# Kernel tuning notes

Measured on AMD Instinct MI355X. Metric: run time of the kernel, lower is better.

Reference implementation:

```python
import jax, jax.numpy as jnp
import numpy as np

D_MODEL = 1024
D_INNER = 4096   # expand=4
D_STATE = 16
D_CONV = 4
DT_RANK = 64     # ceil(d_model/16)
BATCH = 2
SEQLEN = 2048


def setup_inputs() -> dict:
    key = jax.random.key(0)
    ks = jax.random.split(key, 9)
    s = 0.02
    x = jax.random.normal(ks[0], (BATCH, SEQLEN, D_MODEL), jnp.float32)
    in_proj_w = jax.random.normal(ks[1], (D_MODEL, 2 * D_INNER), jnp.float32) * s
    conv_w = jax.random.normal(ks[2], (D_INNER, D_CONV), jnp.float32) * 0.3
    conv_b = jax.random.normal(ks[3], (D_INNER,), jnp.float32) * 0.02
    x_proj_w = jax.random.normal(ks[4], (D_INNER, DT_RANK + 2 * D_STATE), jnp.float32) * s
    dt_proj_w = jax.random.normal(ks[5], (DT_RANK, D_INNER), jnp.float32) * (DT_RANK ** -0.5)
    dt_proj_b = jax.random.normal(ks[6], (D_INNER,), jnp.float32) * 0.1 - 4.0  # small softplus(dt)
    # A = repeat(arange(1, d_state+1)) as in mamba-ssm; A_log = log(A)
    A_log = jnp.log(jnp.broadcast_to(jnp.arange(1, D_STATE + 1, dtype=jnp.float32), (D_INNER, D_STATE)))
    D = jnp.ones((D_INNER,), jnp.float32)
    out_proj_w = jax.random.normal(ks[7], (D_INNER, D_MODEL), jnp.float32) * s
    return {"x": x, "in_proj_w": in_proj_w, "conv_w": conv_w, "conv_b": conv_b,
            "x_proj_w": x_proj_w, "dt_proj_w": dt_proj_w, "dt_proj_b": dt_proj_b,
            "A_log": A_log, "D": D, "out_proj_w": out_proj_w}


def reference(x, in_proj_w, conv_w, conv_b, x_proj_w, dt_proj_w, dt_proj_b, A_log, D, out_proj_w):
    Bsz, L, _ = x.shape
    # input projection -> (x branch, gate z), each [B, L, d_inner]
    xz = x @ in_proj_w
    xc, z = jnp.split(xz, 2, axis=-1)
    # causal depthwise conv1d, kernel D_CONV, left-padded
    xp = jnp.pad(xc, ((0, 0), (D_CONV - 1, 0), (0, 0)))
    xconv = conv_b + sum(xp[:, k:k + L, :] * conv_w[:, k] for k in range(D_CONV))
    xs = jax.nn.silu(xconv)  # [B, L, d_inner]
    # input-dependent SSM params
    proj = xs @ x_proj_w  # [B, L, dt_rank + 2*d_state]
    dt_lo, Bt, Ct = jnp.split(proj, [DT_RANK, DT_RANK + D_STATE], axis=-1)
    dt = jax.nn.softplus(dt_lo @ dt_proj_w + dt_proj_b)  # [B, L, d_inner]
    A = -jnp.exp(A_log)  # [d_inner, d_state]

    def step(h, inp):
        dt_t, B_t, C_t, u_t = inp  # [B,dI], [B,dS], [B,dS], [B,dI]
        dA = jnp.exp(dt_t[..., None] * A)                       # [B, dI, dS]
        h = h * dA + (dt_t * u_t)[..., None] * B_t[:, None, :]  # [B, dI, dS]
        y = jnp.einsum('bdn,bn->bd', h, C_t)                    # [B, dI]
        return h, y

    h0 = jnp.zeros((Bsz, D_INNER, D_STATE), x.dtype)
    inps = (dt.transpose(1, 0, 2), Bt.transpose(1, 0, 2),
            Ct.transpose(1, 0, 2), xs.transpose(1, 0, 2))
    _, ys = jax.lax.scan(step, h0, inps)  # ys: [L, B, d_inner]
    y = ys.transpose(1, 0, 2) + xs * D
    y = y * jax.nn.silu(z)
    return y @ out_proj_w
```

## Files before the change

kernel.cpp:

```cpp
#include <hip/hip_runtime.h>
#include <hip/hip_bf16.h>

#define D_MODEL 1024
#define D_INNER 4096
#define D_STATE 16
#define D_CONV 4
#define DT_RANK 64
#define BATCH 2
#define SEQLEN 2048
#define MROWS (BATCH * SEQLEN)
#define NPROJ (DT_RANK + 2 * D_STATE)
#define PST 128
#define NC 32
#define TC (SEQLEN / NC)
#define KSPLIT 8
#define KSP6 4

typedef unsigned short u16;
typedef unsigned int u32;
typedef __attribute__((ext_vector_type(8))) short short8;
typedef __attribute__((ext_vector_type(4))) float floatx4;

#define LOG2E 1.44269504089f

__device__ __forceinline__ float bf2f(u16 u) {
    union { u32 i; float f; } v; v.i = ((u32)u) << 16; return v.f;
}
__device__ __forceinline__ u16 f2bf(float f) {
    union { float f; u32 i; } v; v.f = f;
    u32 x = v.i;
    u32 r = x + 0x7fffu + ((x >> 16) & 1u);
    return (u16)(r >> 16);
}
__device__ __forceinline__ float softplus_fast(float x) {
    float l = __logf(1.f + __expf(-fabsf(x)));
    return x > 0.f ? x + l : l;
}
__device__ __forceinline__ float sigmoid_fast(float x) {
    return __builtin_amdgcn_rcpf(1.f + __expf(-x));
}
__device__ __forceinline__ float exp2_hw(float x) {
    float r;
    asm("v_exp_f32 %0, %1" : "=v"(r) : "v"(x));
    return r;
}
__device__ __forceinline__ void pow_tree16(float r, float* pw) {
    pw[0] = r;
    pw[1] = r * r;
    pw[2] = pw[1] * r;
    pw[3] = pw[1] * pw[1];
    pw[4] = pw[3] * r;
    pw[5] = pw[3] * pw[1];
    pw[6] = pw[3] * pw[2];
    pw[7] = pw[3] * pw[3];
#pragma unroll
    for (int k = 0; k < 8; k++) pw[8 + k] = pw[7] * pw[k];
}
__device__ __forceinline__ void async_cp16(const u16* g, u16* l) {
    __builtin_amdgcn_global_load_lds((const __attribute__((address_space(1))) void*)g,
                                     (__attribute__((address_space(3))) void*)l, 16, 0, 0);
}

__global__ __launch_bounds__(256) void detect_dtype(const u16* __restrict__ x, int* __restrict__ flag,
                                                    int* __restrict__ sflag) {
    __shared__ int cnt;
    if (threadIdx.x == 0) { cnt = 0; *sflag = 0; }
    __syncthreads();
    int local = 0;
    for (int k = 0; k < 16; k++) {
        int e = threadIdx.x * 8192 + k * 512;
        u16 v = x[2 * e];
        int ex = (v >> 7) & 0xFF;
        if (ex >= 0x68 && ex <= 0x8F) local++;
    }
    atomicAdd(&cnt, local);
    __syncthreads();
    if (threadIdx.x == 0) *flag = (cnt >= 2458) ? 1 : 0;
}

__global__ __launch_bounds__(256) void ingest16(const void* __restrict__ src, u16* __restrict__ dst,
                                                int n, const int* __restrict__ flag) {
    int i = blockIdx.x * 256 + threadIdx.x;
    if (i >= n) return;
    if (*flag) dst[i] = ((const u16*)src)[i];
    else       dst[i] = f2bf(((const float*)src)[i]);
}

__global__ __launch_bounds__(256) void prep_small(const void* __restrict__ cw, const void* __restrict__ cb,
                                                  const void* __restrict__ dtb, const void* __restrict__ Dv,
                                                  const void* __restrict__ Alog,
                                                  u16* __restrict__ cw16, u16* __restrict__ cb16,
                                                  u16* __restrict__ dtb16, u16* __restrict__ D16,
                                                  float* __restrict__ A, const int* __restrict__ flag,
                                                  int* __restrict__ sflag) {
    int i = blockIdx.x * 256 + threadIdx.x;
    int isb = *flag;
    if (i < D_INNER * D_CONV)
        cw16[i] = isb ? ((const u16*)cw)[i] : f2bf(((const float*)cw)[i]);
    if (i < D_INNER) {
        cb16[i]  = isb ? ((const u16*)cb)[i]  : f2bf(((const float*)cb)[i]);
        dtb16[i] = isb ? ((const u16*)dtb)[i] : f2bf(((const float*)dtb)[i]);
        D16[i]   = isb ? ((const u16*)Dv)[i]  : f2bf(((const float*)Dv)[i]);
    }
    if (i < D_INNER * D_STATE) {
        float v = isb ? bf2f(((const u16*)Alog)[i]) : ((const float*)Alog)[i];
        float a = -expf(v);
        A[i] = a;
        float tgt = (float)((i & 15) + 1);
        if (fabsf(a + tgt) > 4e-6f * tgt) atomicOr(sflag, 1);
    }
}

__global__ __launch_bounds__(256) void transpose_w(const void* __restrict__ W, u16* __restrict__ WT,
                                                   int K, int N, const int* __restrict__ flag) {
    __shared__ float t[32][33];
    int k0 = blockIdx.y * 32, n0 = blockIdx.x * 32;
    int tid = threadIdx.x;
    int r = tid >> 3, c4 = (tid & 7) * 4;
    int isb = *flag;
    size_t base = (size_t)(k0 + r) * N + n0 + c4;
    float4 v;
    if (isb) { ushort4 u4 = *(const ushort4*)((const u16*)W + base);
               v = make_float4(bf2f(u4.x), bf2f(u4.y), bf2f(u4.z), bf2f(u4.w)); }
    else     { v = *(const float4*)((const float*)W + base); }
    t[c4 + 0][r] = v.x; t[c4 + 1][r] = v.y; t[c4 + 2][r] = v.z; t[c4 + 3][r] = v.w;
    __syncthreads();
    u16* o = WT + (size_t)(n0 + r) * K + k0 + c4;
    o[0] = f2bf(t[r][c4 + 0]);
    o[1] = f2bf(t[r][c4 + 1]);
    o[2] = f2bf(t[r][c4 + 2]);
    o[3] = f2bf(t[r][c4 + 3]);
}

template<int KS, int MODE>
__global__ __launch_bounds__(512, 2) void gemm8p(const u16* __restrict__ A, const u16* __restrict__ Bt,
                                                 u16* __restrict__ o0, u16* __restrict__ o1,
                                                 float* __restrict__ Pp) {
    __shared__ __align__(16) u16 lds[65536];
    const int tid = threadIdx.x;
    const int lane = tid & 63;
    const int wave = tid >> 6;
    const int wr = wave >> 2, wc = wave & 3;
    const int quad = lane >> 4, l15 = lane & 15;

    int m0, n0, kbase, kz;
    if (MODE == 0) {
        int wgid = (blockIdx.x & 7) * 64 + (blockIdx.x >> 3);
        m0 = (wgid & 15) * 256;
        n0 = (wgid >> 4) * 256;
        kbase = 0; kz = 0;
    } else {
        m0 = blockIdx.y * 256;
        n0 = blockIdx.x * 256;
        kz = blockIdx.z;
        kbase = kz * 1024;
    }
    const int NT = 1024 / 64;

    const int srow = tid >> 3;
    const int kswz = (((tid & 7) ^ (srow & 7)) << 3);
    const u16* pA = A + (size_t)(m0 + srow) * KS + kbase + kswz;
    const u16* pB = Bt + (size_t)(n0 + srow) * KS + kbase + kswz;

    const int rsw = (l15 & 7) << 3;
    const int ksel0 = (quad * 8) ^ rsw;
    const int ksel1 = (32 + quad * 8) ^ rsw;
    const int aoff = (wr * 64 + l15) * 64;
    const int boff = (wc * 32 + l15) * 64;

    floatx4 acc[8][4];
#pragma unroll
    for (int i = 0; i < 8; i++)
#pragma unroll
        for (int j = 0; j < 4; j++) acc[i][j] = (floatx4)0.f;
    short8 af[4][2];
    short8 bf[2][2][2];

#define STAGE_A(nb, h, kt) do { \
    const u16* g_ = pA + (size_t)(h) * 128 * KS + (kt) * 64; \
    u16* l_ = &lds[((nb) * 2 + (h)) * 8192 + tid * 8]; \
    async_cp16(g_, l_); \
    async_cp16(g_ + (size_t)64 * KS, l_ + 4096); \
} while (0)
#define STAGE_B(nb, h, kt) do { \
    const u16* g_ = pB + (size_t)(h) * 128 * KS + (kt) * 64; \
    u16* l_ = &lds[32768 + ((nb) * 2 + (h)) * 8192 + tid * 8]; \
    async_cp16(g_, l_); \
    async_cp16(g_ + (size_t)64 * KS, l_ + 4096); \
} while (0)
#define LOADA(b, h) do { \
    const u16* p_ = &lds[((b) * 2 + (h)) * 8192 + aoff]; \
    _Pragma("unroll") \
    for (int ii = 0; ii < 4; ii++) { \
        af[ii][0] = *(const short8*)(p_ + ii * 1024 + ksel0); \
        af[ii][1] = *(const short8*)(p_ + ii * 1024 + ksel1); \
    } \
} while (0)
#define LOADB(b, h) do { \
    const u16* p_ = &lds[32768 + ((b) * 2 + (h)) * 8192 + boff]; \
    _Pragma("unroll") \
    for (int jj = 0; jj < 2; jj++) { \
        bf[h][jj][0] = *(const short8*)(p_ + jj * 1024 + ksel0); \
        bf[h][jj][1] = *(const short8*)(p_ + jj * 1024 + ksel1); \
    } \
} while (0)
#define MFMAQ(qa, qb) do { \
    __builtin_amdgcn_s_setprio(1); \
    _Pragma("unroll") \
    for (int ii = 0; ii < 4; ii++) \
    _Pragma("unroll") \
    for (int jj = 0; jj < 2; jj++) { \
        floatx4 c_ = acc[(qa) * 4 + ii][(qb) * 2 + jj]; \
        c_ = __builtin_amdgcn_mfma_f32_16x16x32_bf16(af[ii][0], bf[qb][jj][0], c_, 0, 0, 0); \
        c_ = __builtin_amdgcn_mfma_f32_16x16x32_bf16(af[ii][1], bf[qb][jj][1], c_, 0, 0, 0); \
        acc[(qa) * 4 + ii][(qb) * 2 + jj] = c_; \
    } \
    __builtin_amdgcn_s_setprio(0); \
} while (0)
#define VMW(N) asm volatile("s_waitcnt vmcnt(" #N ")" ::: "memory")
#define BARX() do { __builtin_amdgcn_s_barrier(); asm volatile("" ::: "memory"); } while (0)
#define SANDWICH() do { \
    __builtin_amdgcn_sched_barrier(0); \
    __builtin_amdgcn_s_barrier(); \
    asm volatile("s_waitcnt lgkmcnt(0)" ::: "memory"); \
    __builtin_amdgcn_sched_barrier(0); \
} while (0)

    STAGE_A(0, 0, 0);
    STAGE_B(0, 0, 0);
    STAGE_B(0, 1, 0);
    STAGE_A(0, 1, 0);
    VMW(4); BARX();

    for (int t = 0; t < NT - 1; ++t) {
        const int b = t & 1, nb = b ^ 1;
        LOADA(b, 0);
        LOADB(b, 0);
        STAGE_A(nb, 0, t + 1);
        SANDWICH();
        MFMAQ(0, 0);
        VMW(4); BARX();
        LOADB(b, 1);
        STAGE_B(nb, 0, t + 1);
        SANDWICH();
        MFMAQ(0, 1);
        VMW(4); BARX();
        LOADA(b, 1);
        STAGE_B(nb, 1, t + 1);
        SANDWICH();
        MFMAQ(1, 1);
        STAGE_A(nb, 1, t + 1);
        MFMAQ(1, 0);
        VMW(4); BARX();
    }
    {
        const int b = (NT - 1) & 1;
        LOADA(b, 0);
        LOADB(b, 0);
        SANDWICH();
        MFMAQ(0, 0);
        VMW(2); BARX();
        LOADB(b, 1);
        SANDWICH();
        MFMAQ(0, 1);
        VMW(0); BARX();
        LOADA(b, 1);
        MFMAQ(1, 1);
        MFMAQ(1, 0);
    }

    if constexpr (MODE == 0) {
        (void)kz; (void)Pp;
        u16* d = (n0 < D_INNER) ? o0 : o1;
        const int nb0 = (n0 < D_INNER) ? n0 : n0 - D_INNER;
#pragma unroll
        for (int i = 0; i < 8; i++) {
            const int mrow = m0 + wr * 64 + (i & 3) * 16 + (i >> 2) * 128 + quad * 4;
#pragma unroll
            for (int j = 0; j < 4; j++) {
                const int ncol = nb0 + wc * 32 + (j & 1) * 16 + (j >> 1) * 128 + l15;
#pragma unroll
                for (int r = 0; r < 4; r++)
                    d[(size_t)(mrow + r) * D_INNER + ncol] = f2bf(acc[i][j][r]);
            }
        }
    } else {
        (void)o0; (void)o1;
        float* d = Pp + (size_t)kz * MROWS * D_MODEL;
#pragma unroll
        for (int i = 0; i < 8; i++) {
            const int mrow = m0 + wr * 64 + (i & 3) * 16 + (i >> 2) * 128 + quad * 4;
#pragma unroll
            for (int j = 0; j < 4; j++) {
                const int ncol = n0 + wc * 32 + (j & 1) * 16 + (j >> 1) * 128 + l15;
#pragma unroll
                for (int r = 0; r < 4; r++)
                    d[(size_t)(mrow + r) * D_MODEL + ncol] = acc[i][j][r];
            }
        }
    }
#undef STAGE_A
#undef STAGE_B
#undef LOADA
#undef LOADB
#undef MFMAQ
#undef VMW
#undef BARX
#undef SANDWICH
}

__global__ __launch_bounds__(256) void reduce_out(const float* __restrict__ Pp, void* __restrict__ out,
                                                  const int* __restrict__ flag) {
    int i = blockIdx.x * 256 + threadIdx.x;
    float s = 0.f;
#pragma unroll
    for (int z = 0; z < KSP6; z++) s += Pp[(size_t)z * MROWS * D_MODEL + i];
    if (*flag) ((u16*)out)[i] = f2bf(s);
    else       ((float*)out)[i] = s;
}

__global__ __launch_bounds__(256) void gemm_proj(const u16* __restrict__ A, const u16* __restrict__ Bt,
                                                 float* __restrict__ Pp) {
    const int K = D_INNER;
    __shared__ __align__(16) u16 sA[128 * 32];
    __shared__ __align__(16) u16 sB[128 * 32];
    int tid = threadIdx.x;
    int lane = tid & 63;
    int wave = tid >> 6;
    int wm = (wave >> 1) * 64, wn = (wave & 1) * 64;
    int quad = lane >> 4, l15 = lane & 15;
    int m0 = blockIdx.y * 128;
    int kz = blockIdx.x;
    int kbase = kz * (K / KSPLIT);

    floatx4 acc[4][4];
#pragma unroll
    for (int i = 0; i < 4; i++)
#pragma unroll
        for (int j = 0; j < 4; j++) acc[i][j] = (floatx4)0.f;

    const u16* ga0 = A + (size_t)(m0 + (tid >> 2)) * K + (tid & 3) * 8;
    const u16* ga1 = A + (size_t)(m0 + 64 + (tid >> 2)) * K + (tid & 3) * 8;
    const u16* gb0 = Bt + (size_t)(tid >> 2) * K + (tid & 3) * 8;
    const u16* gb1 = Bt + (size_t)(64 + (tid >> 2)) * K + (tid & 3) * 8;
    u16* la0 = &sA[tid * 8];
    u16* la1 = &sA[(256 + tid) * 8];
    u16* lb0 = &sB[tid * 8];
    u16* lb1 = &sB[(256 + tid) * 8];

    for (int k0 = kbase; k0 < kbase + K / KSPLIT; k0 += 32) {
        async_cp16(ga0 + k0, la0);
        async_cp16(ga1 + k0, la1);
        async_cp16(gb0 + k0, lb0);
        async_cp16(gb1 + k0, lb1);
        __syncthreads();
        short8 af[4], bf[4];
#pragma unroll
        for (int i = 0; i < 4; i++) {
            af[i] = *(const short8*)&sA[(wm + i * 16 + l15) * 32 + quad * 8];
            bf[i] = *(const short8*)&sB[(wn + i * 16 + l15) * 32 + quad * 8];
        }
#pragma unroll
        for (int i = 0; i < 4; i++)
#pragma unroll
            for (int j = 0; j < 4; j++)
                acc[i][j] = __builtin_amdgcn_mfma_f32_16x16x32_bf16(af[i], bf[j], acc[i][j], 0, 0, 0);
        __syncthreads();
    }

    float* d = Pp + (size_t)kz * MROWS * PST;
#pragma unroll
    for (int i = 0; i < 4; i++)
#pragma unroll
        for (int j = 0; j < 4; j++)
#pragma unroll
            for (int r = 0; r < 4; r++) {
                int mm = m0 + wm + i * 16 + quad * 4 + r;
                int nn = wn + j * 16 + l15;
                d[(size_t)mm * PST + nn] = acc[i][j][r];
            }
}

__global__ __launch_bounds__(256) void reduce_proj(const float* __restrict__ Pp, float* __restrict__ proj,
                                                   u16* __restrict__ proj_lo) {
    int i = blockIdx.x * 256 + threadIdx.x;
    float s = 0.f;
#pragma unroll
    for (int z = 0; z < KSPLIT; z++) s += Pp[(size_t)z * MROWS * PST + i];
    proj[i] = s;
    int col = i & (PST - 1);
    if (col < DT_RANK) proj_lo[(size_t)(i >> 7) * DT_RANK + col] = f2bf(s);
}

__global__ __launch_bounds__(256) void gemm_dt(const u16* __restrict__ A, const u16* __restrict__ Bt,
                                               const u16* __restrict__ dtb, u16* __restrict__ dt) {
    const int K = DT_RANK;
    __shared__ __align__(16) u16 smem[64 * 132];
    u16* sA = smem;
    u16* sB = smem + 128 * 32;
    int tid = threadIdx.x;
    int lane = tid & 63;
    int wave = tid >> 6;
    int wm = (wave >> 1) * 64, wn = (wave & 1) * 64;
    int quad = lane >> 4, l15 = lane & 15;
    int m0 = blockIdx.y * 128, n0 = blockIdx.x * 128;

    floatx4 acc[4][4];
#pragma unroll
    for (int i = 0; i < 4; i++)
#pragma unroll
        for (int j = 0; j < 4; j++) acc[i][j] = (floatx4)0.f;

    const u16* ga0 = A + (size_t)(m0 + (tid >> 2)) * K + (tid & 3) * 8;
    const u16* ga1 = A + (size_t)(m0 + 64 + (tid >> 2)) * K + (tid & 3) * 8;
    const u16* gb0 = Bt + (size_t)(n0 + (tid >> 2)) * K + (tid & 3) * 8;
    const u16* gb1 = Bt + (size_t)(n0 + 64 + (tid >> 2)) * K + (tid & 3) * 8;
    u16* la0 = &sA[tid * 8];
    u16* la1 = &sA[(256 + tid) * 8];
    u16* lb0 = &sB[tid * 8];
    u16* lb1 = &sB[(256 + tid) * 8];

    for (int k0 = 0; k0 < K; k0 += 32) {
        async_cp16(ga0 + k0, la0);
        async_cp16(ga1 + k0, la1);
        async_cp16(gb0 + k0, lb0);
        async_cp16(gb1 + k0, lb1);
        __syncthreads();
        short8 af[4], bf[4];
#pragma unroll
        for (int i = 0; i < 4; i++) {
            af[i] = *(const short8*)&sA[(wm + i * 16 + l15) * 32 + quad * 8];
            bf[i] = *(const short8*)&sB[(wn + i * 16 + l15) * 32 + quad * 8];
        }
#pragma unroll
        for (int i = 0; i < 4; i++)
#pragma unroll
            for (int j = 0; j < 4; j++)
                acc[i][j] = __builtin_amdgcn_mfma_f32_16x16x32_bf16(af[i], bf[j], acc[i][j], 0, 0, 0);
        __syncthreads();
    }

#pragma unroll
    for (int h = 0; h < 2; h++) {
        __syncthreads();
        if (wm == h * 64) {
#pragma unroll
            for (int j = 0; j < 4; j++) {
                int col = wn + j * 16 + l15;
                float b = bf2f(dtb[n0 + col]);
#pragma unroll
                for (int i = 0; i < 4; i++)
#pragma unroll
                    for (int r = 0; r < 4; r++) {
                        int row = i * 16 + quad * 4 + r;
                        smem[row * 132 + col] = f2bf(softplus_fast(acc[i][j][r] + b));
                    }
            }
        }
        __syncthreads();
#pragma unroll
        for (int p = 0; p < 4; p++) {
            int row = p * 16 + (tid >> 4);
            int chunk = tid & 15;
            uint4 v = *(const uint4*)&smem[row * 132 + chunk * 8];
            *(uint4*)&dt[(size_t)(m0 + h * 64 + row) * D_INNER + n0 + chunk * 8] = v;
        }
    }
}

__global__ __launch_bounds__(256) void conv_silu(const u16* __restrict__ xc, const u16* __restrict__ cw,
                                                 const u16* __restrict__ cb, u16* __restrict__ xs) {
    int idx = blockIdx.x * 256 + threadIdx.x;
    int d = idx & (D_INNER - 1);
    int t = (idx >> 12) & (SEQLEN - 1);
    int b = idx >> 23;
    float w0 = bf2f(cw[d * 4 + 0]), w1 = bf2f(cw[d * 4 + 1]);
    float w2 = bf2f(cw[d * 4 + 2]), w3 = bf2f(cw[d * 4 + 3]);
    float acc = bf2f(cb[d]);
    size_t base = (size_t)b * SEQLEN * D_INNER + d;
    if (t >= 3) acc += bf2f(xc[base + (size_t)(t - 3) * D_INNER]) * w0;
    if (t >= 2) acc += bf2f(xc[base + (size_t)(t - 2) * D_INNER]) * w1;
    if (t >= 1) acc += bf2f(xc[base + (size_t)(t - 1) * D_INNER]) * w2;
    acc += bf2f(xc[base + (size_t)t * D_INNER]) * w3;
    xs[idx] = f2bf(acc * sigmoid_fast(acc));
}

__global__ __launch_bounds__(256) void scan_phase1(const float* __restrict__ proj, const u16* __restrict__ dt,
                                                   const float* __restrict__ A, const u16* __restrict__ xs,
                                                   float* __restrict__ hloc, float* __restrict__ Ssum,
                                                   const int* __restrict__ sflag) {
    int d = blockIdx.x * 256 + threadIdx.x;
    int c = blockIdx.y, b = blockIdx.z;
    int t0 = c * TC;
    int structured = (*sflag == 0);
    float h[16];
#pragma unroll
    for (int n = 0; n < 16; n++) h[n] = 0.f;
    float S = 0.f;
    size_t base = ((size_t)b * SEQLEN + t0) * D_INNER + d;
    const float* prow = proj + ((size_t)b * SEQLEN + t0) * PST + DT_RANK;
    u16 dcur = dt[base], ucur = xs[base];
    if (structured) {
        for (int t = 0; t < TC; t++) {
            size_t nidx = base + (size_t)((t + 1 < TC) ? t + 1 : t) * D_INNER;
            u16 dnxt = dt[nidx];
            u16 unxt = xs[nidx];
            float4 B0 = *(const float4*)(prow + t * PST + 0);
            float4 B1 = *(const float4*)(prow + t * PST + 4);
            float4 B2 = *(const float4*)(prow + t * PST + 8);
            float4 B3 = *(const float4*)(prow + t * PST + 12);
            float dtv = bf2f(dcur), u = bf2f(ucur);
            S += dtv;
            float du = dtv * u;
            float Bf[16] = {B0.x, B0.y, B0.z, B0.w, B1.x, B1.y, B1.z, B1.w,
                            B2.x, B2.y, B2.z, B2.w, B3.x, B3.y, B3.z, B3.w};
            float pw[16];
            pow_tree16(exp2_hw(-LOG2E * dtv), pw);
#pragma unroll
            for (int n = 0; n < 16; n++)
                h[n] = h[n] * pw[n] + du * Bf[n];
            dcur = dnxt; ucur = unxt;
        }
    } else {
        float Areg[16];
        const float4* Ap = (const float4*)(A + (size_t)d * 16);
#pragma unroll
        for (int n = 0; n < 4; n++) {
            float4 v = Ap[n];
            Areg[n * 4 + 0] = v.x * LOG2E; Areg[n * 4 + 1] = v.y * LOG2E;
            Areg[n * 4 + 2] = v.z * LOG2E; Areg[n * 4 + 3] = v.w * LOG2E;
        }
        for (int t = 0; t < TC; t++) {
            size_t nidx = base + (size_t)((t + 1 < TC) ? t + 1 : t) * D_INNER;
            u16 dnxt = dt[nidx];
            u16 unxt = xs[nidx];
            float4 B0 = *(const float4*)(prow + t * PST + 0);
            float4 B1 = *(const float4*)(prow + t * PST + 4);
            float4 B2 = *(const float4*)(prow + t * PST + 8);
            float4 B3 = *(const float4*)(prow + t * PST + 12);
            float dtv = bf2f(dcur), u = bf2f(ucur);
            S += dtv;
            float du = dtv * u;
            float Bf[16] = {B0.x, B0.y, B0.z, B0.w, B1.x, B1.y, B1.z, B1.w,
                            B2.x, B2.y, B2.z, B2.w, B3.x, B3.y, B3.z, B3.w};
#pragma unroll
            for (int n = 0; n < 16; n++)
                h[n] = h[n] * exp2_hw(dtv * Areg[n]) + du * Bf[n];
            dcur = dnxt; ucur = unxt;
        }
    }
    float* hp = &hloc[(((size_t)b * NC + c) * D_INNER + d) * 16];
#pragma unroll
    for (int n = 0; n < 16; n += 4)
        *(float4*)&hp[n] = make_float4(h[n], h[n + 1], h[n + 2], h[n + 3]);
    Ssum[((size_t)b * NC + c) * D_INNER + d] = S;
}

__global__ __launch_bounds__(256) void scan_phase2(const float* __restrict__ A, const float* __restrict__ Ssum,
                                                   float* __restrict__ hloc) {
    int tid = blockIdx.x * 256 + threadIdx.x;
    int n = tid & 15;
    int d = (tid >> 4) & (D_INNER - 1);
    int b = tid >> 16;
    float An2 = A[d * 16 + n] * LOG2E;
    float h = 0.f;
    for (int c = 0; c < NC; c++) {
        size_t idx = (((size_t)b * NC + c) * D_INNER + d) * 16 + n;
        float hl = hloc[idx];
        float S = Ssum[((size_t)b * NC + c) * D_INNER + d];
        hloc[idx] = h;
        h = hl + h * exp2_hw(An2 * S);
    }
}

__global__ __launch_bounds__(256) void scan_phase3(const float* __restrict__ proj, const u16* __restrict__ dt,
                                                   const float* __restrict__ A, const u16* __restrict__ D16,
                                                   const float* __restrict__ hinit, const u16* __restrict__ z16,
                                                   u16* __restrict__ xs, const int* __restrict__ sflag) {
    int d = blockIdx.x * 256 + threadIdx.x;
    int c = blockIdx.y, b = blockIdx.z;
    int t0 = c * TC;
    int structured = (*sflag == 0);
    float h[16];
    {
        const float* hp = &hinit[(((size_t)b * NC + c) * D_INNER + d) * 16];
#pragma unroll
        for (int n = 0; n < 16; n += 4) {
            float4 v = *(const float4*)&hp[n];
            h[n] = v.x; h[n + 1] = v.y; h[n + 2] = v.z; h[n + 3] = v.w;
        }
    }
    float Dd = bf2f(D16[d]);
    size_t base = ((size_t)b * SEQLEN + t0) * D_INNER + d;
    const float* prow = proj + ((size_t)b * SEQLEN + t0) * PST + DT_RANK;
    u16 dcur = dt[base], ucur = xs[base], zcur = z16[base];
    if (structured) {
        for (int t = 0; t < TC; t++) {
            size_t nidx = base + (size_t)((t + 1 < TC) ? t + 1 : t) * D_INNER;
            u16 dnxt = dt[nidx];
            u16 unxt = xs[nidx];
            u16 znxt = z16[nidx];
            float4 B0 = *(const float4*)(prow + t * PST + 0);
            float4 B1 = *(const float4*)(prow + t * PST + 4);
            float4 B2 = *(const float4*)(prow + t * PST + 8);
            float4 B3 = *(const float4*)(prow + t * PST + 12);
            float4 C0 = *(const float4*)(prow + t * PST + 16);
            float4 C1 = *(const float4*)(prow + t * PST + 20);
            float4 C2 = *(const float4*)(prow + t * PST + 24);
            float4 C3 = *(const float4*)(prow + t * PST + 28);
            float dtv = bf2f(dcur), u = bf2f(ucur), zv = bf2f(zcur);
            float du = dtv * u;
            float Bf[16] = {B0.x, B0.y, B0.z, B0.w, B1.x, B1.y, B1.z, B1.w,
                            B2.x, B2.y, B2.z, B2.w, B3.x, B3.y, B3.z, B3.w};
            float Cf[16] = {C0.x, C0.y, C0.z, C0.w, C1.x, C1.y, C1.z, C1.w,
                            C2.x, C2.y, C2.z, C2.w, C3.x, C3.y, C3.z, C3.w};
            float pw[16];
            pow_tree16(exp2_hw(-LOG2E * dtv), pw);
            float y = 0.f;
#pragma unroll
            for (int n = 0; n < 16; n++) {
                h[n] = h[n] * pw[n] + du * Bf[n];
                y += h[n] * Cf[n];
            }
            float gate = zv * sigmoid_fast(zv);
            xs[base + (size_t)t * D_INNER] = f2bf((y + u * Dd) * gate);
            dcur = dnxt; ucur = unxt; zcur = znxt;
        }
    } else {
        float Areg[16];
        const float4* Ap = (const float4*)(A + (size_t)d * 16);
#pragma unroll
        for (int n = 0; n < 4; n++) {
            float4 v = Ap[n];
            Areg[n * 4 + 0] = v.x * LOG2E; Areg[n * 4 + 1] = v.y * LOG2E;
            Areg[n * 4 + 2] = v.z * LOG2E; Areg[n * 4 + 3] = v.w * LOG2E;
        }
        for (int t = 0; t < TC; t++) {
            size_t nidx = base + (size_t)((t + 1 < TC) ? t + 1 : t) * D_INNER;
            u16 dnxt = dt[nidx];
            u16 unxt = xs[nidx];
            u16 znxt = z16[nidx];
            float4 B0 = *(const float4*)(prow + t * PST + 0);
            float4 B1 = *(const float4*)(prow + t * PST + 4);
            float4 B2 = *(const float4*)(prow + t * PST + 8);
            float4 B3 = *(const float4*)(prow + t * PST + 12);
            float4 C0 = *(const float4*)(prow + t * PST + 16);
            float4 C1 = *(const float4*)(prow + t * PST + 20);
            float4 C2 = *(const float4*)(prow + t * PST + 24);
            float4 C3 = *(const float4*)(prow + t * PST + 28);
            float dtv = bf2f(dcur), u = bf2f(ucur), zv = bf2f(zcur);
            float du = dtv * u;
            float Bf[16] = {B0.x, B0.y, B0.z, B0.w, B1.x, B1.y, B1.z, B1.w,
                            B2.x, B2.y, B2.z, B2.w, B3.x, B3.y, B3.z, B3.w};
            float Cf[16] = {C0.x, C0.y, C0.z, C0.w, C1.x, C1.y, C1.z, C1.w,
                            C2.x, C2.y, C2.z, C2.w, C3.x, C3.y, C3.z, C3.w};
            float y = 0.f;
#pragma unroll
            for (int n = 0; n < 16; n++) {
                h[n] = h[n] * exp2_hw(dtv * Areg[n]) + du * Bf[n];
                y += h[n] * Cf[n];
            }
            float gate = zv * sigmoid_fast(zv);
            xs[base + (size_t)t * D_INNER] = f2bf((y + u * Dd) * gate);
            dcur = dnxt; ucur = unxt; zcur = znxt;
        }
    }
}

extern "C" void kernel_launch(void* const* d_in, const int* in_sizes, int n_in,
                              void* d_out, int out_size, void* d_ws, size_t ws_size,
                              hipStream_t stream) {
    const void* x          = d_in[0];
    const void* in_proj_w  = d_in[1];
    const void* conv_w     = d_in[2];
    const void* conv_b     = d_in[3];
    const void* x_proj_w   = d_in[4];
    const void* dt_proj_w  = d_in[5];
    const void* dt_proj_b  = d_in[6];
    const void* A_log      = d_in[7];
    const void* Dvec       = d_in[8];
    const void* out_proj_w = d_in[9];

    char* w = (char*)d_ws;
    const size_t MB = 1024 * 1024;
    const size_t KB = 1024;
    int*   flag    = (int*)(w + 0);
    int*   sflag   = (int*)(w + 16);
    float* Aws     = (float*)(w + 1 * KB);
    float* proj    = (float*)(w + 1 * MB);
    u16*   cw16    = (u16*)(w + 3 * MB);
    u16*   cb16    = (u16*)(w + 3 * MB + 64 * KB);
    u16*   dtb16   = (u16*)(w + 3 * MB + 128 * KB);
    u16*   D16     = (u16*)(w + 3 * MB + 192 * KB);
    u16*   proj_lo = (u16*)(w + 3 * MB + 512 * KB);
    u16*   dtwT    = (u16*)(w + 4 * MB);
    u16*   buf1    = (u16*)(w + 5 * MB);
    u16*   dt16    = buf1;
    u16*   zbuf    = (u16*)(w + 37 * MB);
    float* Pp6     = (float*)(w + 5 * MB);
    u16*   xs      = (u16*)(w + 69 * MB);
    u16*   x16     = (u16*)(w + 101 * MB);
    u16*   ipwT    = (u16*)(w + 110 * MB);
    float* Pp      = (float*)(w + 101 * MB);
    float* hloc    = (float*)(w + 101 * MB);
    float* Ssum    = (float*)(w + 117 * MB);
    u16*   opwT    = (u16*)(w + 127 * MB);
    u16*   xpwT    = (u16*)(w + 136 * MB);

    detect_dtype<<<dim3(1), dim3(256), 0, stream>>>((const u16*)x, flag, sflag);
    prep_small<<<dim3(256), dim3(256), 0, stream>>>(conv_w, conv_b, dt_proj_b, Dvec, A_log,
                                                    cw16, cb16, dtb16, D16, Aws, flag, sflag);
    ingest16<<<dim3(MROWS * D_MODEL / 256), dim3(256), 0, stream>>>(x, x16, MROWS * D_MODEL, flag);
    transpose_w<<<dim3(2 * D_INNER / 32, D_MODEL / 32), dim3(256), 0, stream>>>(in_proj_w, ipwT, D_MODEL, 2 * D_INNER, flag);
    transpose_w<<<dim3(D_MODEL / 32, D_INNER / 32), dim3(256), 0, stream>>>(out_proj_w, opwT, D_INNER, D_MODEL, flag);
    transpose_w<<<dim3(NPROJ / 32, D_INNER / 32), dim3(256), 0, stream>>>(x_proj_w, xpwT, D_INNER, NPROJ, flag);
    transpose_w<<<dim3(D_INNER / 32, DT_RANK / 32), dim3(256), 0, stream>>>(dt_proj_w, dtwT, DT_RANK, D_INNER, flag);

    gemm8p<1024, 0><<<dim3(512), dim3(512), 0, stream>>>(x16, ipwT, buf1, zbuf, nullptr);
    conv_silu<<<dim3(MROWS * D_INNER / 256), dim3(256), 0, stream>>>(buf1, cw16, cb16, xs);
    gemm_proj<<<dim3(KSPLIT, MROWS / 128), dim3(256), 0, stream>>>(xs, xpwT, Pp);
    reduce_proj<<<dim3(MROWS * PST / 256), dim3(256), 0, stream>>>(Pp, proj, proj_lo);
    gemm_dt<<<dim3(D_INNER / 128, MROWS / 128), dim3(256), 0, stream>>>(proj_lo, dtwT, dtb16, dt16);
    scan_phase1<<<dim3(D_INNER / 256, NC, BATCH), dim3(256), 0, stream>>>(proj, dt16, Aws, xs, hloc, Ssum, sflag);
    scan_phase2<<<dim3(BATCH * D_INNER * D_STATE / 256), dim3(256), 0, stream>>>(Aws, Ssum, hloc);
    scan_phase3<<<dim3(D_INNER / 256, NC, BATCH), dim3(256), 0, stream>>>(proj, dt16, Aws, D16, hloc, zbuf, xs, sflag);
    gemm8p<4096, 1><<<dim3(D_MODEL / 256, MROWS / 256, KSP6), dim3(512), 0, stream>>>(xs, opwT, nullptr, nullptr, Pp6);
    reduce_out<<<dim3(MROWS * D_MODEL / 256), dim3(256), 0, stream>>>(Pp6, d_out, flag);
}
```

Before: 461.1 us.

## Switch GEMM to 32x32x16 MFMA and vectorize conv and reduce kernels

The main GEMM kernel now uses 32x32x16 bf16 MFMA instructions with 16-float accumulators instead of 16x16x32, so each wave needs fewer LDS fragment loads per unit of compute. The LDS fragment addressing and epilogue index mapping are rewritten to match the new instruction layout. Separately, conv_silu now handles 8 channels per thread with 128-bit loads and stores, and reduce_out processes 4 elements per thread with float4 accesses. The new layout carries a risk of indexing errors, and the epilogue stores stay strided per lane.

```diff
diff --git a/kernel.cpp b/kernel.cpp
--- a/kernel.cpp
+++ b/kernel.cpp
@@ -20,6 +20,7 @@
 typedef unsigned int u32;
 typedef __attribute__((ext_vector_type(8))) short short8;
 typedef __attribute__((ext_vector_type(4))) float floatx4;
+typedef __attribute__((ext_vector_type(16))) float floatx16;
 
 #define LOG2E 1.44269504089f
 
@@ -141,7 +142,7 @@
     const int lane = tid & 63;
     const int wave = tid >> 6;
     const int wr = wave >> 2, wc = wave & 3;
-    const int quad = lane >> 4, l15 = lane & 15;
+    const int l31 = lane & 31, lhi = lane >> 5, sw = lane & 7;
 
     int m0, n0, kbase, kz;
     if (MODE == 0) {
@@ -162,19 +163,20 @@
     const u16* pA = A + (size_t)(m0 + srow) * KS + kbase + kswz;
     const u16* pB = Bt + (size_t)(n0 + srow) * KS + kbase + kswz;
 
-    const int rsw = (l15 & 7) << 3;
-    const int ksel0 = (quad * 8) ^ rsw;
-    const int ksel1 = (32 + quad * 8) ^ rsw;
-    const int aoff = (wr * 64 + l15) * 64;
-    const int boff = (wc * 32 + l15) * 64;
-
-    floatx4 acc[8][4];
-#pragma unroll
-    for (int i = 0; i < 8; i++)
-#pragma unroll
-        for (int j = 0; j < 4; j++) acc[i][j] = (floatx4)0.f;
-    short8 af[4][2];
-    short8 bf[2][2][2];
+    const int k0f = (((0 + lhi) ^ sw) << 3);
+    const int k1f = (((2 + lhi) ^ sw) << 3);
+    const int k2f = (((4 + lhi) ^ sw) << 3);
+    const int k3f = (((6 + lhi) ^ sw) << 3);
+    const int aoff = (wr * 64 + l31) * 64;
+    const int boff = (wc * 32 + l31) * 64;
+
+    floatx16 acc[4][2];
+#pragma unroll
+    for (int i = 0; i < 4; i++)
+#pragma unroll
+        for (int j = 0; j < 2; j++) acc[i][j] = (floatx16)0.f;
+    short8 af[2][4];
+    short8 bfr[2][4];
 
 #define STAGE_A(nb, h, kt) do { \
     const u16* g_ = pA + (size_t)(h) * 128 * KS + (kt) * 64; \
@@ -190,30 +192,32 @@
 } while (0)
 #define LOADA(b, h) do { \
     const u16* p_ = &lds[((b) * 2 + (h)) * 8192 + aoff]; \
-    _Pragma("unroll") \
-    for (int ii = 0; ii < 4; ii++) { \
-        af[ii][0] = *(const short8*)(p_ + ii * 1024 + ksel0); \
-        af[ii][1] = *(const short8*)(p_ + ii * 1024 + ksel1); \
-    } \
+    af[0][0] = *(const short8*)(p_ + k0f); \
+    af[0][1] = *(const short8*)(p_ + k1f); \
+    af[0][2] = *(const short8*)(p_ + k2f); \
+    af[0][3] = *(const short8*)(p_ + k3f); \
+    af[1][0] = *(const short8*)(p_ + 2048 + k0f); \
+    af[1][1] = *(const short8*)(p_ + 2048 + k1f); \
+    af[1][2] = *(const short8*)(p_ + 2048 + k2f); \
+    af[1][3] = *(const short8*)(p_ + 2048 + k3f); \
 } while (0)
 #define LOADB(b, h) do { \
     const u16* p_ = &lds[32768 + ((b) * 2 + (h)) * 8192 + boff]; \
-    _Pragma("unroll") \
-    for (int jj = 0; jj < 2; jj++) { \
-        bf[h][jj][0] = *(const short8*)(p_ + jj * 1024 + ksel0); \
-        bf[h][jj][1] = *(const short8*)(p_ + jj * 1024 + ksel1); \
-    } \
+    bfr[h][0] = *(const short8*)(p_ + k0f); \
+    bfr[h][1] = *(const short8*)(p_ + k1f); \
+    bfr[h][2] = *(const short8*)(p_ + k2f); \
+    bfr[h][3] = *(const short8*)(p_ + k3f); \
 } while (0)
 #define MFMAQ(qa, qb) do { \
     __builtin_amdgcn_s_setprio(1); \
     _Pragma("unroll") \
-    for (int ii = 0; ii < 4; ii++) \
-    _Pragma("unroll") \
-    for (int jj = 0; jj < 2; jj++) { \
-        floatx4 c_ = acc[(qa) * 4 + ii][(qb) * 2 + jj]; \
-        c_ = __builtin_amdgcn_mfma_f32_16x16x32_bf16(af[ii][0], bf[qb][jj][0], c_, 0, 0, 0); \
-        c_ = __builtin_amdgcn_mfma_f32_16x16x32_bf16(af[ii][1], bf[qb][jj][1], c_, 0, 0, 0); \
-        acc[(qa) * 4 + ii][(qb) * 2 + jj] = c_; \
+    for (int ii = 0; ii < 2; ii++) { \
+        floatx16 c_ = acc[(qa) * 2 + ii][qb]; \
+        c_ = __builtin_amdgcn_mfma_f32_32x32x16_bf16(af[ii][0], bfr[qb][0], c_, 0, 0, 0); \
+        c_ = __builtin_amdgcn_mfma_f32_32x32x16_bf16(af[ii][1], bfr[qb][1], c_, 0, 0, 0); \
+        c_ = __builtin_amdgcn_mfma_f32_32x32x16_bf16(af[ii][2], bfr[qb][2], c_, 0, 0, 0); \
+        c_ = __builtin_amdgcn_mfma_f32_32x32x16_bf16(af[ii][3], bfr[qb][3], c_, 0, 0, 0); \
+        acc[(qa) * 2 + ii][qb] = c_; \
     } \
     __builtin_amdgcn_s_setprio(0); \
 } while (0)
@@ -274,28 +278,32 @@
         u16* d = (n0 < D_INNER) ? o0 : o1;
         const int nb0 = (n0 < D_INNER) ? n0 : n0 - D_INNER;
 #pragma unroll
-        for (int i = 0; i < 8; i++) {
-            const int mrow = m0 + wr * 64 + (i & 3) * 16 + (i >> 2) * 128 + quad * 4;
-#pragma unroll
-            for (int j = 0; j < 4; j++) {
-                const int ncol = nb0 + wc * 32 + (j & 1) * 16 + (j >> 1) * 128 + l15;
-#pragma unroll
-                for (int r = 0; r < 4; r++)
-                    d[(size_t)(mrow + r) * D_INNER + ncol] = f2bf(acc[i][j][r]);
+        for (int i = 0; i < 4; i++) {
+            const int rbase = m0 + (i >> 1) * 128 + wr * 64 + (i & 1) * 32 + lhi * 4;
+#pragma unroll
+            for (int j = 0; j < 2; j++) {
+                const int ncol = nb0 + j * 128 + wc * 32 + l31;
+#pragma unroll
+                for (int reg = 0; reg < 16; reg++) {
+                    const int row = rbase + (reg & 3) + ((reg >> 2) << 3);
+                    d[(size_t)row * D_INNER + ncol] = f2bf(acc[i][j][reg]);
+                }
             }
         }
     } else {
         (void)o0; (void)o1;
         float* d = Pp + (size_t)kz * MROWS * D_MODEL;
 #pragma unroll
-        for (int i = 0; i < 8; i++) {
-            const int mrow = m0 + wr * 64 + (i & 3) * 16 + (i >> 2) * 128 + quad * 4;
-#pragma unroll
-            for (int j = 0; j < 4; j++) {
-                const int ncol = n0 + wc * 32 + (j & 1) * 16 + (j >> 1) * 128 + l15;
-#pragma unroll
-                for (int r = 0; r < 4; r++)
-                    d[(size_t)(mrow + r) * D_MODEL + ncol] = acc[i][j][r];
+        for (int i = 0; i < 4; i++) {
+            const int rbase = m0 + (i >> 1) * 128 + wr * 64 + (i & 1) * 32 + lhi * 4;
+#pragma unroll
+            for (int j = 0; j < 2; j++) {
+                const int ncol = n0 + j * 128 + wc * 32 + l31;
+#pragma unroll
+                for (int reg = 0; reg < 16; reg++) {
+                    const int row = rbase + (reg & 3) + ((reg >> 2) << 3);
+                    d[(size_t)row * D_MODEL + ncol] = acc[i][j][reg];
+                }
             }
         }
     }
@@ -311,12 +319,19 @@
 
 __global__ __launch_bounds__(256) void reduce_out(const float* __restrict__ Pp, void* __restrict__ out,
                                                   const int* __restrict__ flag) {
-    int i = blockIdx.x * 256 + threadIdx.x;
-    float s = 0.f;
-#pragma unroll
-    for (int z = 0; z < KSP6; z++) s += Pp[(size_t)z * MROWS * D_MODEL + i];
-    if (*flag) ((u16*)out)[i] = f2bf(s);
-    else       ((float*)out)[i] = s;
+    int i = (blockIdx.x * 256 + threadIdx.x) * 4;
+    float4 s = *(const float4*)&Pp[i];
+#pragma unroll
+    for (int z = 1; z < KSP6; z++) {
+        float4 p = *(const float4*)&Pp[(size_t)z * MROWS * D_MODEL + i];
+        s.x += p.x; s.y += p.y; s.z += p.z; s.w += p.w;
+    }
+    if (*flag) {
+        ushort4 o = make_ushort4(f2bf(s.x), f2bf(s.y), f2bf(s.z), f2bf(s.w));
+        *(ushort4*)((u16*)out + i) = o;
+    } else {
+        *(float4*)((float*)out + i) = s;
+    }
 }
 
 __global__ __launch_bounds__(256) void gemm_proj(const u16* __restrict__ A, const u16* __restrict__ Bt,
@@ -471,18 +486,37 @@
 __global__ __launch_bounds__(256) void conv_silu(const u16* __restrict__ xc, const u16* __restrict__ cw,
                                                  const u16* __restrict__ cb, u16* __restrict__ xs) {
     int idx = blockIdx.x * 256 + threadIdx.x;
-    int d = idx & (D_INNER - 1);
-    int t = (idx >> 12) & (SEQLEN - 1);
-    int b = idx >> 23;
-    float w0 = bf2f(cw[d * 4 + 0]), w1 = bf2f(cw[d * 4 + 1]);
-    float w2 = bf2f(cw[d * 4 + 2]), w3 = bf2f(cw[d * 4 + 3]);
-    float acc = bf2f(cb[d]);
-    size_t base = (size_t)b * SEQLEN * D_INNER + d;
-    if (t >= 3) acc += bf2f(xc[base + (size_t)(t - 3) * D_INNER]) * w0;
-    if (t >= 2) acc += bf2f(xc[base + (size_t)(t - 2) * D_INNER]) * w1;
-    if (t >= 1) acc += bf2f(xc[base + (size_t)(t - 1) * D_INNER]) * w2;
-    acc += bf2f(xc[base + (size_t)t * D_INNER]) * w3;
-    xs[idx] = f2bf(acc * sigmoid_fast(acc));
+    int g = idx & (D_INNER / 8 - 1);
+    int bt = idx >> 9;
+    int t = bt & (SEQLEN - 1);
+    int d0 = g * 8;
+    size_t row = (size_t)bt * D_INNER + d0;
+    u16 wv[32];
+    *(uint4*)&wv[0]  = *(const uint4*)&cw[d0 * 4];
+    *(uint4*)&wv[8]  = *(const uint4*)&cw[d0 * 4 + 8];
+    *(uint4*)&wv[16] = *(const uint4*)&cw[d0 * 4 + 16];
+    *(uint4*)&wv[24] = *(const uint4*)&cw[d0 * 4 + 24];
+    u16 cbv[8];
+    *(uint4*)&cbv[0] = *(const uint4*)&cb[d0];
+    u16 x0[8] = {0, 0, 0, 0, 0, 0, 0, 0};
+    u16 x1[8] = {0, 0, 0, 0, 0, 0, 0, 0};
+    u16 x2[8] = {0, 0, 0, 0, 0, 0, 0, 0};
+    u16 x3[8];
+    if (t >= 3) *(uint4*)x0 = *(const uint4*)&xc[row - 3 * (size_t)D_INNER];
+    if (t >= 2) *(uint4*)x1 = *(const uint4*)&xc[row - 2 * (size_t)D_INNER];
+    if (t >= 1) *(uint4*)x2 = *(const uint4*)&xc[row - 1 * (size_t)D_INNER];
+    *(uint4*)x3 = *(const uint4*)&xc[row];
+    u16 out[8];
+#pragma unroll
+    for (int ch = 0; ch < 8; ch++) {
+        float a = bf2f(cbv[ch]);
+        a += bf2f(x0[ch]) * bf2f(wv[ch * 4 + 0]);
+        a += bf2f(x1[ch]) * bf2f(wv[ch * 4 + 1]);
+        a += bf2f(x2[ch]) * bf2f(wv[ch * 4 + 2]);
+        a += bf2f(x3[ch]) * bf2f(wv[ch * 4 + 3]);
+        out[ch] = f2bf(a * sigmoid_fast(a));
+    }
+    *(uint4*)&xs[row] = *(const uint4*)&out[0];
 }
 
 __global__ __launch_bounds__(256) void scan_phase1(const float* __restrict__ proj, const u16* __restrict__ dt,
@@ -717,7 +751,7 @@
     transpose_w<<<dim3(D_INNER / 32, DT_RANK / 32), dim3(256), 0, stream>>>(dt_proj_w, dtwT, DT_RANK, D_INNER, flag);
 
     gemm8p<1024, 0><<<dim3(512), dim3(512), 0, stream>>>(x16, ipwT, buf1, zbuf, nullptr);
-    conv_silu<<<dim3(MROWS * D_INNER / 256), dim3(256), 0, stream>>>(buf1, cw16, cb16, xs);
+    conv_silu<<<dim3(MROWS * D_INNER / 8 / 256), dim3(256), 0, stream>>>(buf1, cw16, cb16, xs);
     gemm_proj<<<dim3(KSPLIT, MROWS / 128), dim3(256), 0, stream>>>(xs, xpwT, Pp);
     reduce_proj<<<dim3(MROWS * PST / 256), dim3(256), 0, stream>>>(Pp, proj, proj_lo);
     gemm_dt<<<dim3(D_INNER / 128, MROWS / 128), dim3(256), 0, stream>>>(proj_lo, dtwT, dtb16, dt16);
@@ -725,5 +759,5 @@
     scan_phase2<<<dim3(BATCH * D_INNER * D_STATE / 256), dim3(256), 0, stream>>>(Aws, Ssum, hloc);
     scan_phase3<<<dim3(D_INNER / 256, NC, BATCH), dim3(256), 0, stream>>>(proj, dt16, Aws, D16, hloc, zbuf, xs, sflag);
     gemm8p<4096, 1><<<dim3(D_MODEL / 256, MROWS / 256, KSP6), dim3(512), 0, stream>>>(xs, opwT, nullptr, nullptr, Pp6);
-    reduce_out<<<dim3(MROWS * D_MODEL / 256), dim3(256), 0, stream>>>(Pp6, d_out, flag);
-}
+    reduce_out<<<dim3(MROWS * D_MODEL / 1024), dim3(256), 0, stream>>>(Pp6, d_out, flag);
+}
```

Measured after the change: 430.4 us. -6.7%, faster.
